# Kernel optimization log

Hardware: AMD Instinct MI355X
Metric: run time of the kernel (lower is better)

## Reference

```python
import jax, jax.numpy as jnp
import numpy as np

PAD_IDX, BOS_IDX, EOS_IDX = 0, 1, 2
NUM_LABELS = 48
B, T = 1024, 512
NEG = -10000.0


def make_trans(key):
    trans = jax.random.normal(key, (NUM_LABELS, NUM_LABELS), dtype=jnp.float32)
    trans = trans.at[BOS_IDX, :].set(NEG)
    trans = trans.at[:, EOS_IDX].set(NEG)
    trans = trans.at[:, PAD_IDX].set(NEG)
    trans = trans.at[PAD_IDX, :].set(NEG)
    trans = trans.at[PAD_IDX, EOS_IDX].set(0.0)
    trans = trans.at[PAD_IDX, PAD_IDX].set(0.0)
    return trans


def setup_inputs() -> dict:
    key = jax.random.key(0)
    k_h, k_tr = jax.random.split(key)
    h = jax.random.normal(k_h, (B, T, NUM_LABELS), dtype=jnp.float32)
    mask = jnp.ones((B, T), dtype=jnp.float32)
    trans = make_trans(k_tr)
    return {"h": h, "mask": mask, "trans": trans, "batch_size": B}


def reference(h, mask, trans, batch_size):
    # h: (B, T, L), mask: (B, T), trans: (L, L)
    L = trans.shape[0]
    score0 = jnp.full((batch_size, L), NEG, dtype=h.dtype).at[:, BOS_IDX].set(0.0)

    def step(score, inp):
        h_t, m_t = inp            # h_t: (B, L), m_t: (B,)
        # new[b, i] = logsumexp_j(score[b, j] + h_t[b, i] + trans[i, j])
        z = score[:, None, :] + h_t[:, :, None] + trans[None, :, :]  # (B, L, L)
        score_t = jax.nn.logsumexp(z, axis=-1)
        m = m_t[:, None]
        score = score_t * m + score * (1.0 - m)
        return score, None

    # scan over time: move T to leading axis
    score, _ = jax.lax.scan(step, score0, (jnp.swapaxes(h, 0, 1), jnp.swapaxes(mask, 0, 1)))
    return jax.nn.logsumexp(score, axis=-1)  # (B,)
```

## Files before the change

### kernel.cpp

```cpp
#include <hip/hip_runtime.h>
#include <math.h>

typedef float f32x2 __attribute__((ext_vector_type(2)));
typedef float f32x4 __attribute__((ext_vector_type(4)));

namespace {
constexpr int L = 48;
constexpr int OCT = 8;
constexpr float LN2f = 0.69314718055994530942f;
}

__global__ __launch_bounds__(64, 1)
void crf_fwd(const float* __restrict__ h,
             const float* __restrict__ mask,
             const float* __restrict__ trans,
             float* __restrict__ out, int T) {
  const int b = blockIdx.x;
  const int lane = threadIdx.x;
  const bool active = lane < L;
  const int safelane = active ? lane : 0;

  __shared__ __align__(16) float p_lds[64];

  f32x2 Ep[L / 2];
  if (active) {
#pragma unroll
    for (int k = 0; k < L / 2; ++k) {
      Ep[k].x = __expf(trans[lane * L + 2 * k]);
      Ep[k].y = __expf(trans[lane * L + 2 * k + 1]);
    }
  } else {
#pragma unroll
    for (int k = 0; k < L / 2; ++k) Ep[k] = (f32x2){0.f, 0.f};
  }

  float p = (lane == 1) ? 1.0f : 0.0f;
  p_lds[lane] = p;
  int Mi = 0;
  float rs = 1.0f;

  const float* __restrict__ hb = h + (size_t)b * T * L;
  const float* __restrict__ mb = mask + (size_t)b * T;
  const int NOCT = T / OCT;

  float hf[OCT], mf[OCT];
#pragma unroll
  for (int k = 0; k < OCT; ++k) {
    hf[k] = hb[k * L + safelane];
    mf[k] = mb[k];
  }

  for (int oct = 0; oct < NOCT; ++oct) {
    float hn[OCT], mn[OCT];
    if (oct + 1 < NOCT) {
      const float* nb = hb + (size_t)(oct + 1) * OCT * L;
#pragma unroll
      for (int k = 0; k < OCT; ++k) {
        hn[k] = nb[k * L + safelane];
        mn[k] = mb[(oct + 1) * OCT + k];
      }
    } else {
#pragma unroll
      for (int k = 0; k < OCT; ++k) { hn[k] = 0.f; mn[k] = 1.f; }
    }

#pragma unroll
    for (int tt = 0; tt < OCT; ++tt) {
      const bool RENORM = ((tt & 3) == 3);
      float g  = __expf(hf[tt]) * rs;
      float pr = p * rs;
      rs = 1.0f;

      const f32x4* p4 = reinterpret_cast<const f32x4*>(p_lds);
      f32x4 w0 = p4[0], w1 = p4[1];
      f32x2 a0 = w0.xy * Ep[0], a1 = w0.zw * Ep[1];
      f32x2 a2 = w1.xy * Ep[2], a3 = w1.zw * Ep[3];
      f32x4 w6s = w0, w7s = w0, w8s = w0, w9s = w0;
#pragma unroll
      for (int k = 2; k < 12; ++k) {
        f32x4 t = p4[k];
        if (k & 1) { a2 += t.xy * Ep[2 * k]; a3 += t.zw * Ep[2 * k + 1]; }
        else       { a0 += t.xy * Ep[2 * k]; a1 += t.zw * Ep[2 * k + 1]; }
        if (RENORM) {
          if (k == 6) w6s = t;
          if (k == 7) w7s = t;
          if (k == 8) w8s = t;
          if (k == 9) w9s = t;
        }
      }
      f32x2 sc = (a0 + a1) + (a2 + a3);
      float s = sc.x + sc.y;
      float pn = s * g;
      p = (mf[tt] > 0.5f) ? pn : pr;
      p_lds[lane] = p;

      if (RENORM) {
        float ma = fmaxf(fmaxf(w6s.x, w6s.y), fmaxf(w6s.z, w6s.w));
        float mb2 = fmaxf(fmaxf(w7s.x, w7s.y), fmaxf(w7s.z, w7s.w));
        float mc = fmaxf(fmaxf(w8s.x, w8s.y), fmaxf(w8s.z, w8s.w));
        float md = fmaxf(fmaxf(w9s.x, w9s.y), fmaxf(w9s.z, w9s.w));
        float mx = fmaxf(fmaxf(ma, mb2), fmaxf(mc, md));
        unsigned bits = __float_as_uint(mx);
        int ke = (int)(bits >> 23) & 0xFF;
        bool ok = (ke > 0) && (ke < 255);
        rs = ok ? __uint_as_float((unsigned)(254 - ke) << 23) : 1.0f;
        Mi += ok ? (ke - 127) : 0;
      }
    }
#pragma unroll
    for (int k = 0; k < OCT; ++k) { hf[k] = hn[k]; mf[k] = mn[k]; }
  }

  float ps = p;
#pragma unroll
  for (int off = 32; off; off >>= 1) ps += __shfl_xor(ps, off, 64);
  if (lane == 0) out[b] = ((float)Mi + __log2f(ps)) * LN2f;
}

extern "C" void kernel_launch(void* const* d_in, const int* in_sizes, int n_in,
                              void* d_out, int out_size, void* d_ws, size_t ws_size,
                              hipStream_t stream) {
  const float* h     = (const float*)d_in[0];
  const float* mask  = (const float*)d_in[1];
  const float* trans = (const float*)d_in[2];
  float* out = (float*)d_out;
  const int B = out_size;
  const int T = in_sizes[1] / B;
  crf_fwd<<<B, 64, 0, stream>>>(h, mask, trans, out, T);
}
```

Before: 252.3 us.

## Broadcast probabilities via readlane instead of LDS round-trip

Each step now broadcasts the previous probability vector from lanes with 48 scalar readlane operations instead of writing it to LDS and reading it back as vectors. Each product becomes a scalar FMA with an SGPR operand. The renormalisation max now covers all 48 entries, compared as unsigned integers on the raw bits, where before it looked at a 16-entry subset. This removes the LDS write/read latency from the serial recurrence, but it turns packed f32x2 math into scalar FMAs and adds 48 readlane instructions per step.

```diff
diff --git a/kernel.cpp b/kernel.cpp
--- a/kernel.cpp
+++ b/kernel.cpp
@@ -1,8 +1,5 @@
 #include <hip/hip_runtime.h>
 #include <math.h>
-
-typedef float f32x2 __attribute__((ext_vector_type(2)));
-typedef float f32x4 __attribute__((ext_vector_type(4)));
 
 namespace {
 constexpr int L = 48;
@@ -20,22 +17,16 @@
   const bool active = lane < L;
   const int safelane = active ? lane : 0;
 
-  __shared__ __align__(16) float p_lds[64];
-
-  f32x2 Ep[L / 2];
+  float E[L];
   if (active) {
 #pragma unroll
-    for (int k = 0; k < L / 2; ++k) {
-      Ep[k].x = __expf(trans[lane * L + 2 * k]);
-      Ep[k].y = __expf(trans[lane * L + 2 * k + 1]);
-    }
+    for (int j = 0; j < L; ++j) E[j] = __expf(trans[lane * L + j]);
   } else {
 #pragma unroll
-    for (int k = 0; k < L / 2; ++k) Ep[k] = (f32x2){0.f, 0.f};
+    for (int j = 0; j < L; ++j) E[j] = 0.0f;
   }
 
   float p = (lane == 1) ? 1.0f : 0.0f;
-  p_lds[lane] = p;
   int Mi = 0;
   float rs = 1.0f;
 
@@ -71,38 +62,35 @@
       float pr = p * rs;
       rs = 1.0f;
 
-      const f32x4* p4 = reinterpret_cast<const f32x4*>(p_lds);
-      f32x4 w0 = p4[0], w1 = p4[1];
-      f32x2 a0 = w0.xy * Ep[0], a1 = w0.zw * Ep[1];
-      f32x2 a2 = w1.xy * Ep[2], a3 = w1.zw * Ep[3];
-      f32x4 w6s = w0, w7s = w0, w8s = w0, w9s = w0;
+      const int pb = __float_as_int(p);
+      float a0 = 0.f, a1 = 0.f, a2 = 0.f, a3 = 0.f;
+      unsigned mx = 0u;
 #pragma unroll
-      for (int k = 2; k < 12; ++k) {
-        f32x4 t = p4[k];
-        if (k & 1) { a2 += t.xy * Ep[2 * k]; a3 += t.zw * Ep[2 * k + 1]; }
-        else       { a0 += t.xy * Ep[2 * k]; a1 += t.zw * Ep[2 * k + 1]; }
+      for (int j = 0; j < L; j += 4) {
+        const int r0 = __builtin_amdgcn_readlane(pb, j + 0);
+        const int r1 = __builtin_amdgcn_readlane(pb, j + 1);
+        const int r2 = __builtin_amdgcn_readlane(pb, j + 2);
+        const int r3 = __builtin_amdgcn_readlane(pb, j + 3);
+        a0 = fmaf(__int_as_float(r0), E[j + 0], a0);
+        a1 = fmaf(__int_as_float(r1), E[j + 1], a1);
+        a2 = fmaf(__int_as_float(r2), E[j + 2], a2);
+        a3 = fmaf(__int_as_float(r3), E[j + 3], a3);
         if (RENORM) {
-          if (k == 6) w6s = t;
-          if (k == 7) w7s = t;
-          if (k == 8) w8s = t;
-          if (k == 9) w9s = t;
+          const unsigned u0 = (unsigned)r0, u1 = (unsigned)r1;
+          const unsigned u2 = (unsigned)r2, u3 = (unsigned)r3;
+          const unsigned m01 = u0 > u1 ? u0 : u1;
+          const unsigned m23 = u2 > u3 ? u2 : u3;
+          const unsigned m03 = m01 > m23 ? m01 : m23;
+          mx = mx > m03 ? mx : m03;
         }
       }
-      f32x2 sc = (a0 + a1) + (a2 + a3);
-      float s = sc.x + sc.y;
-      float pn = s * g;
+      const float s = (a0 + a1) + (a2 + a3);
+      const float pn = s * g;
       p = (mf[tt] > 0.5f) ? pn : pr;
-      p_lds[lane] = p;
 
       if (RENORM) {
-        float ma = fmaxf(fmaxf(w6s.x, w6s.y), fmaxf(w6s.z, w6s.w));
-        float mb2 = fmaxf(fmaxf(w7s.x, w7s.y), fmaxf(w7s.z, w7s.w));
-        float mc = fmaxf(fmaxf(w8s.x, w8s.y), fmaxf(w8s.z, w8s.w));
-        float md = fmaxf(fmaxf(w9s.x, w9s.y), fmaxf(w9s.z, w9s.w));
-        float mx = fmaxf(fmaxf(ma, mb2), fmaxf(mc, md));
-        unsigned bits = __float_as_uint(mx);
-        int ke = (int)(bits >> 23) & 0xFF;
-        bool ok = (ke > 0) && (ke < 255);
+        const int ke = (int)(mx >> 23);
+        const bool ok = (ke > 0) && (ke < 255);
         rs = ok ? __uint_as_float((unsigned)(254 - ke) << 23) : 1.0f;
         Mi += ok ? (ke - 127) : 0;
       }
```

Result: faster. 239.3 us (-5.2%).
